# Optimization experiments

Hardware: AMD Instinct MI355X
Metric: run time of the kernel (lower is better)

Reference implementation:

```python
import jax, jax.numpy as jnp
import numpy as np


def setup_inputs() -> dict:
    key = jax.random.key(0)
    k1, k2 = jax.random.split(key)
    imgs = jax.random.normal(k1, (16, 64, 64, 64), dtype=jnp.float32)
    # matches np.random.normal(0, 0.01, (1, inCs, outCs, filtSize, filtSize, 2))
    filts = 0.01 * jax.random.normal(k2, (1, 64, 64, 3, 3, 2), dtype=jnp.float32)
    return {"imgs": imgs, "filts": filts}


def reference(imgs, filts):
    # imgs:  [B, inC, H, W] real
    # filts: [1, inC, outC, fs, fs, 2] (real/imag planes)
    B, inC, H, W = imgs.shape
    fs = filts.shape[3]
    # zero-pad image to S = H + fs - 1 (full linear-conv FFT size)
    imgs_p = jnp.pad(imgs, ((0, 0), (0, 0), (0, fs - 1), (0, fs - 1)))
    img_f = jnp.fft.fftn(imgs_p, axes=(-2, -1))  # [B, inC, S, S] complex64
    # complex filter, padded to same FFT size
    fc = (filts[0, ..., 0] + 1j * filts[0, ..., 1]).astype(jnp.complex64)  # [inC, outC, fs, fs]
    fc_p = jnp.pad(fc, ((0, 0), (0, 0), (0, H - 1), (0, W - 1)))
    filt_f = jnp.fft.fftn(fc_p, axes=(-2, -1))  # [inC, outC, S, S]
    # Karatsuba complex multiply + sum over inC == complex contraction over inC.
    # Fused as one einsum instead of materializing [B,inC,outC,S,S] intermediates.
    out_f = jnp.einsum('bihw,iohw->bohw', img_f, filt_f)  # [B, outC, S, S]
    out = jnp.fft.ifftn(out_f, axes=(-2, -1))
    # crop [1:-1, 1:-1] and take real part, as in the torch module
    return out[:, :, 1:-1, 1:-1].real.astype(imgs.dtype)
```

## Files before the change

kernel.cpp:

```cpp
#include <hip/hip_runtime.h>


typedef _Float16 f16x8 __attribute__((ext_vector_type(8)));
typedef float    f32x4 __attribute__((ext_vector_type(4)));

#define NB 16
#define NC 64
#define NH 64
#define NW 64
#define CHUNKS 528
#define SLAB_BYTES (CHUNKS * 16)
#define WF_HALFS (9 * 2 * 4 * 64 * 8)

__global__ __launch_bounds__(256) void prep_w(const float* __restrict__ filts,
                                              _Float16* __restrict__ wf) {
    const int f = blockIdx.x * 256 + threadIdx.x;
    if (f >= WF_HALFS) return;
    const int e  = f & 7;
    const int l  = (f >> 3) & 63;
    const int n  = (f >> 9) & 3;
    const int kc = (f >> 11) & 1;
    const int t  = f >> 12;
    const int i  = kc * 32 + (l >> 4) * 8 + e;
    const int o  = n * 16 + (l & 15);
    const int ky = t / 3, kx = t % 3;
    wf[f] = (_Float16)filts[(((i * 64 + o) * 3 + ky) * 3 + kx) * 2];
}

__global__ __launch_bounds__(256, 2) void conv_direct(const float* __restrict__ imgs,
                                                      const _Float16* __restrict__ wf,
                                                      float* __restrict__ out) {
    __shared__ uint4 ldsb[4 * SLAB_BYTES / 16];
    char* lds = reinterpret_cast<char*>(ldsb);
    const int bid = blockIdx.x;
    const int b   = bid >> 5;
    const int y0  = (bid & 31) << 1;
    const int tid = threadIdx.x;
    const int w   = tid >> 6;
    const int l   = tid & 63;
    const int h   = l >> 4;
    const int r   = l & 15;

    {
        const int rs = w;
        const int y  = y0 + rs - 1;
        const bool yv = ((unsigned)y < (unsigned)NH);
        char* slab = lds + rs * SLAB_BYTES;
        #pragma unroll
        for (int ci = 0; ci < 8; ++ci) {
            f16x8 v;
            if (yv) {
                const float* src = imgs + (((size_t)(b * NC + ci * 8)) * NH + y) * NW + l;
                #pragma unroll
                for (int k = 0; k < 8; ++k) v[k] = (_Float16)src[(size_t)k * NH * NW];
            } else {
                #pragma unroll
                for (int k = 0; k < 8; ++k) v[k] = (_Float16)0.f;
            }
            const int xp = l + 1;
            const int chunk = xp * 8 + (ci ^ (xp & 7));
            *reinterpret_cast<f16x8*>(slab + chunk * 16) = v;
            if (l < 2) {
                const int xp2 = l ? 65 : 0;
                const int c2  = xp2 * 8 + (ci ^ (xp2 & 7));
                f16x8 z;
                #pragma unroll
                for (int k = 0; k < 8; ++k) z[k] = (_Float16)0.f;
                *reinterpret_cast<f16x8*>(slab + c2 * 16) = z;
            }
        }
    }
    __syncthreads();

    const int row = w >> 1;
    const int oh  = w & 1;

    f32x4 acc[4][2];
    #pragma unroll
    for (int m = 0; m < 4; ++m)
        #pragma unroll
        for (int n = 0; n < 2; ++n)
            acc[m][n] = f32x4{0.f, 0.f, 0.f, 0.f};

    #pragma unroll
    for (int ky = 0; ky < 3; ++ky) {
        const char* slab = lds + (row + 2 - ky) * SLAB_BYTES;
        #pragma unroll
        for (int kx = 0; kx < 3; ++kx) {
            const _Float16* wft = wf + (size_t)(ky * 3 + kx) * (2 * 4 * 64 * 8);
            #pragma unroll
            for (int kc = 0; kc < 2; ++kc) {
                f16x8 a[4], bb[2];
                #pragma unroll
                for (int m = 0; m < 4; ++m) {
                    const int xp = m * 16 + r + 2 - kx;
                    const int chunk = xp * 8 + (((kc << 2) + h) ^ (xp & 7));
                    a[m] = *reinterpret_cast<const f16x8*>(slab + chunk * 16);
                }
                #pragma unroll
                for (int n = 0; n < 2; ++n)
                    bb[n] = *reinterpret_cast<const f16x8*>(
                        wft + ((size_t)((kc << 2) + (oh * 2 + n)) * 64 + l) * 8);
                #pragma unroll
                for (int m = 0; m < 4; ++m)
                    #pragma unroll
                    for (int n = 0; n < 2; ++n)
                        acc[m][n] = __builtin_amdgcn_mfma_f32_16x16x32_f16(a[m], bb[n], acc[m][n], 0, 0, 0);
            }
        }
    }

    const int y = y0 + row;
    #pragma unroll
    for (int m = 0; m < 4; ++m) {
        const int x0 = m * 16 + h * 4;
        #pragma unroll
        for (int n = 0; n < 2; ++n) {
            const int o = oh * 32 + n * 16 + r;
            *reinterpret_cast<f32x4*>(out + (((size_t)(b * 64 + o) * 64 + y) * 64) + x0) = acc[m][n];
        }
    }
}

extern "C" void kernel_launch(void* const* d_in, const int* in_sizes, int n_in,
                              void* d_out, int out_size, void* d_ws, size_t ws_size,
                              hipStream_t stream) {
    const float* imgs  = (const float*)d_in[0];
    const float* filts = (const float*)d_in[1];
    float* out = (float*)d_out;
    _Float16* wfb = (_Float16*)d_ws;

    hipLaunchKernelGGL(prep_w, dim3((WF_HALFS + 255) / 256), dim3(256), 0, stream, filts, wfb);
    hipLaunchKernelGGL(conv_direct, dim3(NB * 32), dim3(256), 0, stream, imgs, wfb, out);
}
```

Before: 22.54 us.

## Split conv blocks to one output row each with swizzled block order

Each block now computes one output row with two waves covering the 64 output channels, instead of two rows with four waves. The grid doubles to 1024 blocks of 128 threads and the LDS per block shrinks to three input slabs. The block index is swizzled so consecutive blocks spread across batches and rows. This should improve occupancy and load balance across CUs, at the cost of reloading each input row three times instead of two times per pair of output rows.

```diff
diff --git a/kernel.cpp b/kernel.cpp
--- a/kernel.cpp
+++ b/kernel.cpp
@@ -27,53 +27,51 @@
     wf[f] = (_Float16)filts[(((i * 64 + o) * 3 + ky) * 3 + kx) * 2];
 }
 
-__global__ __launch_bounds__(256, 2) void conv_direct(const float* __restrict__ imgs,
-                                                      const _Float16* __restrict__ wf,
-                                                      float* __restrict__ out) {
-    __shared__ uint4 ldsb[4 * SLAB_BYTES / 16];
+__global__ __launch_bounds__(128, 2) void conv_row(const float* __restrict__ imgs,
+                                                   const _Float16* __restrict__ wf,
+                                                   float* __restrict__ out) {
+    __shared__ uint4 ldsb[3 * SLAB_BYTES / 16];
     char* lds = reinterpret_cast<char*>(ldsb);
     const int bid = blockIdx.x;
-    const int b   = bid >> 5;
-    const int y0  = (bid & 31) << 1;
+    const int swz = ((bid & 7) << 7) | (bid >> 3);
+    const int b   = swz >> 6;
+    const int y   = swz & 63;
     const int tid = threadIdx.x;
     const int w   = tid >> 6;
     const int l   = tid & 63;
     const int h   = l >> 4;
     const int r   = l & 15;
 
-    {
-        const int rs = w;
-        const int y  = y0 + rs - 1;
-        const bool yv = ((unsigned)y < (unsigned)NH);
-        char* slab = lds + rs * SLAB_BYTES;
+    if (tid < 48) {
+        const int sl  = tid >> 4;
+        const int rem = tid & 15;
+        const int ci  = rem >> 1;
+        const int xp2 = (rem & 1) ? 65 : 0;
+        const int c2  = xp2 * 8 + (ci ^ (xp2 & 7));
+        f16x8 z;
         #pragma unroll
-        for (int ci = 0; ci < 8; ++ci) {
-            f16x8 v;
-            if (yv) {
-                const float* src = imgs + (((size_t)(b * NC + ci * 8)) * NH + y) * NW + l;
-                #pragma unroll
-                for (int k = 0; k < 8; ++k) v[k] = (_Float16)src[(size_t)k * NH * NW];
-            } else {
-                #pragma unroll
-                for (int k = 0; k < 8; ++k) v[k] = (_Float16)0.f;
-            }
-            const int xp = l + 1;
-            const int chunk = xp * 8 + (ci ^ (xp & 7));
-            *reinterpret_cast<f16x8*>(slab + chunk * 16) = v;
-            if (l < 2) {
-                const int xp2 = l ? 65 : 0;
-                const int c2  = xp2 * 8 + (ci ^ (xp2 & 7));
-                f16x8 z;
-                #pragma unroll
-                for (int k = 0; k < 8; ++k) z[k] = (_Float16)0.f;
-                *reinterpret_cast<f16x8*>(slab + c2 * 16) = z;
-            }
+        for (int k = 0; k < 8; ++k) z[k] = (_Float16)0.f;
+        *reinterpret_cast<f16x8*>(lds + sl * SLAB_BYTES + c2 * 16) = z;
+    }
+
+    for (int g = w; g < 24; g += 2) {
+        const int sl = g >> 3;
+        const int ci = g & 7;
+        const int yy = y - 1 + sl;
+        f16x8 v;
+        if ((unsigned)yy < (unsigned)NH) {
+            const float* src = imgs + (((size_t)(b * NC + ci * 8)) * NH + yy) * NW + l;
+            #pragma unroll
+            for (int k = 0; k < 8; ++k) v[k] = (_Float16)src[(size_t)k * NH * NW];
+        } else {
+            #pragma unroll
+            for (int k = 0; k < 8; ++k) v[k] = (_Float16)0.f;
         }
+        const int xp = l + 1;
+        const int chunk = xp * 8 + (ci ^ (xp & 7));
+        *reinterpret_cast<f16x8*>(lds + sl * SLAB_BYTES + chunk * 16) = v;
     }
     __syncthreads();
-
-    const int row = w >> 1;
-    const int oh  = w & 1;
 
     f32x4 acc[4][2];
     #pragma unroll
@@ -84,7 +82,7 @@
 
     #pragma unroll
     for (int ky = 0; ky < 3; ++ky) {
-        const char* slab = lds + (row + 2 - ky) * SLAB_BYTES;
+        const char* slab = lds + (2 - ky) * SLAB_BYTES;
         #pragma unroll
         for (int kx = 0; kx < 3; ++kx) {
             const _Float16* wft = wf + (size_t)(ky * 3 + kx) * (2 * 4 * 64 * 8);
@@ -100,7 +98,7 @@
                 #pragma unroll
                 for (int n = 0; n < 2; ++n)
                     bb[n] = *reinterpret_cast<const f16x8*>(
-                        wft + ((size_t)((kc << 2) + (oh * 2 + n)) * 64 + l) * 8);
+                        wft + ((size_t)((kc << 2) + (w * 2 + n)) * 64 + l) * 8);
                 #pragma unroll
                 for (int m = 0; m < 4; ++m)
                     #pragma unroll
@@ -110,13 +108,12 @@
         }
     }
 
-    const int y = y0 + row;
     #pragma unroll
     for (int m = 0; m < 4; ++m) {
         const int x0 = m * 16 + h * 4;
         #pragma unroll
         for (int n = 0; n < 2; ++n) {
-            const int o = oh * 32 + n * 16 + r;
+            const int o = w * 32 + n * 16 + r;
             *reinterpret_cast<f32x4*>(out + (((size_t)(b * 64 + o) * 64 + y) * 64) + x0) = acc[m][n];
         }
     }
@@ -131,5 +128,5 @@
     _Float16* wfb = (_Float16*)d_ws;
 
     hipLaunchKernelGGL(prep_w, dim3((WF_HALFS + 255) / 256), dim3(256), 0, stream, filts, wfb);
-    hipLaunchKernelGGL(conv_direct, dim3(NB * 32), dim3(256), 0, stream, imgs, wfb, out);
+    hipLaunchKernelGGL(conv_row, dim3(NB * NH), dim3(128), 0, stream, imgs, wfb, out);
 }
```

Result: no change. 22.50 us (-0.2%).
